# Kernel optimization log

Hardware: AMD Instinct MI355X
Metric: run time of the kernel (lower is better)

Reference implementation:

```python
import jax, jax.numpy as jnp
import numpy as np

SEQ, BATCH = 512, 32
VOCAB, HID, FF = 32000, 1024, 4096
HEADS, NX, MAXLEN = 8, 6, 512
EPS = 1e-5


def _full_layer_norm(t):
    # F.layer_norm(t, t.shape): normalize over ALL elements, no affine
    m = jnp.mean(t)
    v = jnp.mean((t - m) ** 2)
    return (t - m) * jax.lax.rsqrt(v + EPS)


def _attention(x, wq, bq, wk, bk, wv, bv, wo, bo):
    # x: [S, B, H]; faithful to the module's quirky reshape:
    # view(B, S//heads, heads, H) splits the SEQUENCE dim across heads,
    # each head keeps the full feature dim H; scores scaled by sqrt(H//heads).
    S, B, H = x.shape
    head_dim = H // HEADS
    q = x @ wq + bq
    k = x @ wk + bk
    v = x @ wv + bv

    def split(t):  # [S,B,H] -> [B, heads, S//heads, H]
        return t.transpose(1, 0, 2).reshape(B, S // HEADS, HEADS, H).transpose(0, 2, 1, 3)

    qh, kh, vh = split(q), split(k), split(v)
    energy = jnp.einsum('bhtf,bhsf->bhts', qh, kh) / np.sqrt(head_dim)
    att = jax.nn.softmax(energy, axis=-1)          # [B, heads, S//h, S//h]
    va = jnp.einsum('bhts,bhsf->bhtf', att, vh)    # [B, heads, S//h, H]
    va = va.transpose(2, 0, 1, 3).reshape(S, B, H)  # back to [S, B, H]
    return va @ wo + bo


def _sub_encoder(x, p, i):
    a = _attention(x, p['wq'][i], p['bq'][i], p['wk'][i], p['bk'][i],
                   p['wv'][i], p['bv'][i], p['wo'][i], p['bo'][i])
    mid = _full_layer_norm(a + x)
    f = jax.nn.relu(mid @ p['w1'][i] + p['b1'][i]) @ p['w2'][i] + p['b2'][i]
    return _full_layer_norm(mid + f)


def setup_inputs() -> dict:
    key = jax.random.key(0)
    ks = jax.random.split(key, 16)
    s = 0.02
    inp = {
        'x': jax.random.randint(ks[0], (SEQ, BATCH), 0, VOCAB),
        'emb': jax.random.normal(ks[1], (VOCAB, HID), jnp.float32) * s,
        'pos_emb': jax.random.normal(ks[2], (MAXLEN, HID), jnp.float32) * s,
        'wq': jax.random.normal(ks[3], (NX, HID, HID), jnp.float32) * s,
        'bq': jnp.zeros((NX, HID), jnp.float32),
        'wk': jax.random.normal(ks[4], (NX, HID, HID), jnp.float32) * s,
        'bk': jnp.zeros((NX, HID), jnp.float32),
        'wv': jax.random.normal(ks[5], (NX, HID, HID), jnp.float32) * s,
        'bv': jnp.zeros((NX, HID), jnp.float32),
        'wo': jax.random.normal(ks[6], (NX, HID, HID), jnp.float32) * s,
        'bo': jnp.zeros((NX, HID), jnp.float32),
        'w1': jax.random.normal(ks[7], (NX, HID, FF), jnp.float32) * s,
        'b1': jnp.zeros((NX, FF), jnp.float32),
        'w2': jax.random.normal(ks[8], (NX, FF, HID), jnp.float32) * s,
        'b2': jnp.zeros((NX, HID), jnp.float32),
    }
    return inp


def reference(x, emb, pos_emb, wq, bq, wk, bk, wv, bv, wo, bo, w1, b1, w2, b2):
    # dropout layers are identity (eval mode); src_mask=None path
    S = x.shape[0]
    p = dict(wq=wq, bq=bq, wk=wk, bk=bk, wv=wv, bv=bv, wo=wo, bo=bo,
             w1=w1, b1=b1, w2=w2, b2=b2)
    h = emb[x] * np.sqrt(HID) + pos_emb[jnp.arange(S)][:, None, :]
    for i in range(NX):
        h = _sub_encoder(h, p, i)
    return h
```

## Files before the change

### kernel.cpp

```cpp
#include <hip/hip_runtime.h>
#include <hip/hip_bf16.h>
#include <stdint.h>

typedef __bf16 bf16_t;
typedef __bf16 bf16x8 __attribute__((ext_vector_type(8)));
typedef __bf16 bf16x4 __attribute__((ext_vector_type(4)));
typedef float  f32x4  __attribute__((ext_vector_type(4)));
typedef float  f32x16 __attribute__((ext_vector_type(16)));

#define SEQ   512
#define BATCH 32
#define HID   1024
#define FFD   4096
#define NROW  (SEQ*BATCH)
#define NTOT  ((long)NROW*HID)
#define QKVS  3072

typedef __attribute__((address_space(3))) uint32_t lds_u32;
typedef __attribute__((address_space(1))) const uint32_t glb_u32;

__device__ __forceinline__ void gload_lds16(const void* g, void* l) {
  glb_u32* gp = reinterpret_cast<glb_u32*>(reinterpret_cast<uintptr_t>(g));
  lds_u32* lp = reinterpret_cast<lds_u32*>(reinterpret_cast<uintptr_t>(l));
  __builtin_amdgcn_global_load_lds(gp, lp, 16, 0, 0);
}

__global__ __launch_bounds__(256) void embed_k(const int* __restrict__ x,
    const float* __restrict__ emb, const float* __restrict__ pos,
    bf16_t* __restrict__ hb, float* __restrict__ stId)
{
  if (blockIdx.x == 0 && threadIdx.x == 0) { stId[0] = 0.f; stId[1] = 1.f; }
  const long row = blockIdx.x;
  const int  s   = (int)(row >> 5);
  const long idx = x[row];
  const int  t   = threadIdx.x;
  float4 e  = ((const float4*)(emb + idx*HID))[t];
  float4 pv = ((const float4*)(pos + (long)s*HID))[t];
  bf16x4 ob = {(bf16_t)(e.x*32.f+pv.x), (bf16_t)(e.y*32.f+pv.y),
               (bf16_t)(e.z*32.f+pv.z), (bf16_t)(e.w*32.f+pv.w)};
  *(bf16x4*)(hb + row*HID + (long)t*4) = ob;
}

__device__ __forceinline__ void wcvtNL_body(const float* __restrict__ W,
    bf16_t* __restrict__ wT, int K, int N, int bid)
{
  const int t  = threadIdx.x;
  const int nt = N >> 9;
  const int n  = ((bid % nt) << 9) + t;
  const int k0 = (bid / nt) << 6;
#pragma unroll
  for (int kb = 0; kb < 64; kb += 8) {
    bf16x8 o;
#pragma unroll
    for (int j = 0; j < 8; ++j)
      o[j] = (bf16_t)W[(long)(k0 + kb + j)*N + n];
    *(bf16x8*)&wT[(long)n*K + k0 + kb] = o;
  }
}

__device__ __forceinline__ void csum512_body(const float* __restrict__ W,
    float* __restrict__ out, int K, int N, int bid)
{
  const int n = bid*512 + threadIdx.x;
  float s0 = 0.f, s1 = 0.f, s2 = 0.f, s3 = 0.f;
  for (int k = 0; k < K; k += 4) {
    s0 += W[(long)k*N + n];
    s1 += W[(long)(k+1)*N + n];
    s2 += W[(long)(k+2)*N + n];
    s3 += W[(long)(k+3)*N + n];
  }
  out[n] = (s0 + s1) + (s2 + s3);
}

__global__ __launch_bounds__(512) void prep0(const float* __restrict__ wq,
    const float* __restrict__ wk, const float* __restrict__ wv,
    bf16_t* __restrict__ wT3, float* __restrict__ cs3)
{
  const int b = blockIdx.x;
  if (b < 96) {
    const int sel = b >> 5;
    const float* W = sel == 0 ? wq : sel == 1 ? wk : wv;
    wcvtNL_body(W, wT3 + (size_t)sel*HID*HID, HID, HID, b & 31);
  } else {
    const int col = (b - 96)*512 + threadIdx.x;
    const int sel = col >> 10, n = col & 1023;
    const float* W = sel == 0 ? wq : sel == 1 ? wk : wv;
    float s = 0.f;
    for (int k = 0; k < HID; ++k) s += W[(long)k*HID + n];
    cs3[col] = s;
  }
}

__global__ __launch_bounds__(512) void prep_k(
    const float* __restrict__ Wo, bf16_t* __restrict__ wTo,
    const float* __restrict__ W1, bf16_t* __restrict__ wT1, float* __restrict__ cs1,
    const float* __restrict__ W2, bf16_t* __restrict__ wT2,
    const float* __restrict__ Wq, const float* __restrict__ Wk,
    const float* __restrict__ Wv, bf16_t* __restrict__ wT3,
    float* __restrict__ cs3)
{
  const int b = blockIdx.x;
  if (b < 32)        wcvtNL_body(Wo, wTo, HID, HID, b);
  else if (b < 160)  wcvtNL_body(W1, wT1, HID, FFD, b - 32);
  else if (b < 288)  wcvtNL_body(W2, wT2, FFD, HID, b - 160);
  else if (b < 296)  csum512_body(W1, cs1, HID, FFD, b - 288);
  else if (b < 392) {
    const int i = b - 296, sel = i >> 5;
    const float* W = sel == 0 ? Wq : sel == 1 ? Wk : Wv;
    wcvtNL_body(W, wT3 + (size_t)sel*HID*HID, HID, HID, i & 31);
  } else {
    const int col = (b - 392)*512 + threadIdx.x;
    const int sel = col >> 10, n = col & 1023;
    const float* W = sel == 0 ? Wq : sel == 1 ? Wk : Wv;
    float s = 0.f;
    for (int k = 0; k < HID; ++k) s += W[(long)k*HID + n];
    cs3[col] = s;
  }
}

template<int MODE>
__global__ __launch_bounds__(512, 4)
void gemmW(const bf16_t* __restrict__ A, const bf16_t* __restrict__ Bt,
           const float* __restrict__ ba, const float* __restrict__ bb,
           const float* __restrict__ bc, const float* __restrict__ cs,
           const float* __restrict__ stats, const bf16_t* __restrict__ res,
           bf16_t* __restrict__ outB, float* __restrict__ part,
           int M, int N, int K)
{
  __shared__ bf16_t As[128][64];
  __shared__ bf16_t Bs[256][64];
  __shared__ float  rs[512], rq[512];
  const int tid = threadIdx.x;
  const int w = tid >> 6, l = tid & 63;
  const int wm = w >> 2, wn = w & 3;
  const int lr = l & 31, hi = l >> 5;

  const int nbn = N >> 8;
  const int nwg = gridDim.x;
  const int q8 = nwg >> 3, r8 = nwg & 7;
  const int xcd = blockIdx.x & 7, bidx = blockIdx.x >> 3;
  const int wg = (xcd < r8 ? xcd*(q8+1) : r8*(q8+1) + (xcd-r8)*q8) + bidx;
  const long bm = wg / nbn, bn = wg % nbn;
  const long rA0 = bm << 7, rB0 = bn << 8;

  const int srow   = tid >> 3;
  const int schunk = (((tid & 7) ^ ((tid >> 3) & 7)) << 3);
  const int ldsw   = (tid >> 6) << 10;

  f32x16 a00 = {0}, a01 = {0}, a10 = {0}, a11 = {0};

#define STG_TILE(kt) do { \
    const long kb_ = (long)(kt)*64 + schunk; \
    gload_lds16(A  + (rA0 + srow)*(long)K + kb_,        (char*)As + ldsw); \
    gload_lds16(A  + (rA0 + 64 + srow)*(long)K + kb_,   (char*)As + 8192 + ldsw); \
    gload_lds16(Bt + (rB0 + srow)*(long)K + kb_,        (char*)Bs + ldsw); \
    gload_lds16(Bt + (rB0 + 64 + srow)*(long)K + kb_,   (char*)Bs + 8192 + ldsw); \
    gload_lds16(Bt + (rB0 + 128 + srow)*(long)K + kb_,  (char*)Bs + 16384 + ldsw); \
    gload_lds16(Bt + (rB0 + 192 + srow)*(long)K + kb_,  (char*)Bs + 24576 + ldsw); \
  } while (0)
#define FRA(mt, kk) (*(const bf16x8*)((const char*)As + (wm*64 + (mt)*32 + lr)*128 + \
                      ((((kk)*2 + hi) ^ (l & 7)) << 4)))
#define FRB(nt, kk) (*(const bf16x8*)((const char*)Bs + (wn*64 + (nt)*32 + lr)*128 + \
                      ((((kk)*2 + hi) ^ (l & 7)) << 4)))

  const int nk = K >> 6;
  for (int t = 0; t < nk; ++t) {
    __syncthreads();
    STG_TILE(t);
    __syncthreads();
#pragma unroll
    for (int kk = 0; kk < 4; ++kk) {
      bf16x8 fa0 = FRA(0, kk), fa1 = FRA(1, kk);
      bf16x8 fb0 = FRB(0, kk), fb1 = FRB(1, kk);
      a00 = __builtin_amdgcn_mfma_f32_32x32x16_bf16(fa0, fb0, a00, 0, 0, 0);
      a01 = __builtin_amdgcn_mfma_f32_32x32x16_bf16(fa0, fb1, a01, 0, 0, 0);
      a10 = __builtin_amdgcn_mfma_f32_32x32x16_bf16(fa1, fb0, a10, 0, 0, 0);
      a11 = __builtin_amdgcn_mfma_f32_32x32x16_bf16(fa1, fb1, a11, 0, 0, 0);
    }
  }
#undef STG_TILE
#undef FRA
#undef FRB

  const float mS = stats[0], rS = stats[1];
  const bool q3 = (N == 3072);
  float ls = 0.f, lsq = 0.f;
  const long rowT = rA0 + wm*64 + 4*hi;
  const long colT = rB0 + wn*64 + lr;
#pragma unroll
  for (int nt = 0; nt < 2; ++nt) {
    const long col = colT + nt*32;
    float bv;
    if (MODE == 3 && q3)
      bv = col < 1024 ? ba[col] : col < 2048 ? bb[col - 1024] : bc[col - 2048];
    else
      bv = ba[col];
    float beta = 0.f;
    if (MODE == 3 || MODE == 4) beta = bv - mS*rS*cs[col];
#pragma unroll
    for (int mt = 0; mt < 2; ++mt) {
      const f32x16 acc = mt == 0 ? (nt == 0 ? a00 : a01) : (nt == 0 ? a10 : a11);
#pragma unroll
      for (int r = 0; r < 16; ++r) {
        const long row = rowT + mt*32 + (r & 3) + 8*(r >> 2);
        const long off = row*(long)N + col;
        float v;
        if (MODE == 3)      v = fmaf(acc[r], rS, beta);
        else if (MODE == 4) v = fmaxf(fmaf(acc[r], rS, beta), 0.f);
        else {
          v = acc[r] + bv + ((float)res[off] - mS)*rS;
          ls += v; lsq += v*v;
        }
        outB[off] = (bf16_t)v;
      }
    }
  }
  if (MODE == 5) {
    rs[tid] = ls; rq[tid] = lsq;
    __syncthreads();
    for (int o = 256; o > 0; o >>= 1) {
      if (tid < o) { rs[tid] += rs[tid+o]; rq[tid] += rq[tid+o]; }
      __syncthreads();
    }
    if (tid == 0) { part[2*blockIdx.x] = rs[0]; part[2*blockIdx.x + 1] = rq[0]; }
  }
}

__global__ __launch_bounds__(256) void attn_m(
    const bf16_t* __restrict__ qkv, bf16_t* __restrict__ ob)
{
  __shared__ __align__(16) bf16_t QK[2][8192];
  __shared__ __align__(16) bf16_t Ps[64*64];
  bf16_t* Vs = &QK[0][0];
  bf16_t* Os = &QK[1][0];

  const int tid = threadIdx.x;
  const int w = tid >> 6, l = tid & 63;
  const int fr = l & 15, kq = l >> 4;
  const int head = blockIdx.x & 7, b = blockIdx.x >> 3;
  const long rbase = (long)head*32 + b;

  const int lr  = tid >> 2;
  const int sslot = (tid & 15) ^ (tid >> 4);

  f32x4 accS[4] = {{0,0,0,0},{0,0,0,0},{0,0,0,0},{0,0,0,0}};

  for (int kc = 0; kc < HID; kc += 128) {
    __syncthreads();
#pragma unroll
    for (int i = 0; i < 4; ++i) {
      const int r = i*16 + (tid >> 4);
      const long gq = ((long)r*256 + rbase)*QKVS + kc + sslot*8;
      gload_lds16(qkv + gq,        (char*)&QK[0][0] + i*4096 + w*1024);
      gload_lds16(qkv + gq + 1024, (char*)&QK[1][0] + i*4096 + w*1024);
    }
    __syncthreads();
#pragma unroll
    for (int kk = 0; kk < 4; ++kk) {
      const int ra = w*16 + fr;
      bf16x8 a = *(const bf16x8*)&QK[0][ra*128 + (((kk*4 + kq) ^ fr) << 3)];
#pragma unroll
      for (int n = 0; n < 4; ++n) {
        const int rb = n*16 + fr;
        bf16x8 bv = *(const bf16x8*)&QK[1][rb*128 + (((kk*4 + kq) ^ fr) << 3)];
        accS[n] = __builtin_amdgcn_mfma_f32_16x16x32_bf16(a, bv, accS[n], 0, 0, 0);
      }
    }
  }

  const float scale = 0.08838834764831843f;
  float pj[4][4];
#pragma unroll
  for (int j = 0; j < 4; ++j) {
    float m = fmaxf(fmaxf(accS[0][j], accS[1][j]), fmaxf(accS[2][j], accS[3][j]));
    m = fmaxf(m, __shfl_xor(m, 1));
    m = fmaxf(m, __shfl_xor(m, 2));
    m = fmaxf(m, __shfl_xor(m, 4));
    m = fmaxf(m, __shfl_xor(m, 8));
    m *= scale;
    float s = 0.f;
#pragma unroll
    for (int n = 0; n < 4; ++n) { pj[n][j] = __expf(accS[n][j]*scale - m); s += pj[n][j]; }
    s += __shfl_xor(s, 1);
    s += __shfl_xor(s, 2);
    s += __shfl_xor(s, 4);
    s += __shfl_xor(s, 8);
    const float rv = 1.f / s;
#pragma unroll
    for (int n = 0; n < 4; ++n) pj[n][j] *= rv;
  }
#pragma unroll
  for (int n = 0; n < 4; ++n)
#pragma unroll
    for (int j = 0; j < 4; ++j) {
      const int r = w*16 + kq*4 + j;
      const int cpos = n*16 + fr;
      Ps[r*64 + (((cpos >> 3) ^ (r & 7)) << 3) + (cpos & 7)] = (bf16_t)pj[n][j];
    }
  __syncthreads();

  const long orow = (long)lr*256 + b*8 + head;
  for (int fc = 0; fc < HID; fc += 128) {
    const bf16_t* vrow = qkv + ((long)lr*256 + rbase)*QKVS + 2048 + fc;
#pragma unroll
    for (int i = 0; i < 4; ++i) {
      const int f0 = (tid & 3)*8 + i*32;
      uint4 vv = *(const uint4*)&vrow[f0];
      const bf16_t* ve = (const bf16_t*)&vv;
#pragma unroll
      for (int j = 0; j < 8; ++j) {
        const int f = f0 + j;
        Vs[f*64 + (((lr >> 3) ^ (f & 7)) << 3) + (lr & 7)] = ve[j];
      }
    }
    __syncthreads();
    const int ra = w*16 + fr;
    bf16x8 a0 = *(const bf16x8*)&Ps[ra*64 + ((kq       ^ (ra & 7)) << 3)];
    bf16x8 a1 = *(const bf16x8*)&Ps[ra*64 + (((4 + kq) ^ (ra & 7)) << 3)];
    f32x4 accO[8];
#pragma unroll
    for (int nt = 0; nt < 8; ++nt) {
      const int f = nt*16 + fr;
      bf16x8 b0 = *(const bf16x8*)&Vs[f*64 + ((kq       ^ (f & 7)) << 3)];
      bf16x8 b1 = *(const bf16x8*)&Vs[f*64 + (((4 + kq) ^ (f & 7)) << 3)];
      accO[nt] = __builtin_amdgcn_mfma_f32_16x16x32_bf16(a0, b0, (f32x4){0.f,0.f,0.f,0.f}, 0, 0, 0);
      accO[nt] = __builtin_amdgcn_mfma_f32_16x16x32_bf16(a1, b1, accO[nt], 0, 0, 0);
    }
#pragma unroll
    for (int nt = 0; nt < 8; ++nt)
#pragma unroll
      for (int j = 0; j < 4; ++j) {
        const int r = w*16 + kq*4 + j;
        const int cpos = nt*16 + fr;
        Os[r*128 + (((cpos >> 3) ^ (r & 7)) << 3) + (cpos & 7)] = (bf16_t)accO[nt][j];
      }
    __syncthreads();
#pragma unroll
    for (int i = 0; i < 4; ++i) {
      const int p = (tid & 3)*4 + i;
      uint4 vv = *(const uint4*)&Os[lr*128 + ((p ^ (lr & 7)) << 3)];
      *(uint4*)&ob[orow*HID + fc + p*8] = vv;
    }
  }
}

__global__ __launch_bounds__(256) void reduce2(const float* __restrict__ part,
                                               float* __restrict__ stats, int np)
{
  __shared__ double sh[256], sh2[256];
  const int tid = threadIdx.x;
  double s = 0.0, s2 = 0.0;
  for (int i = tid; i < np; i += 256) { s += part[2*i]; s2 += part[2*i + 1]; }
  sh[tid] = s; sh2[tid] = s2; __syncthreads();
  for (int o = 128; o > 0; o >>= 1) {
    if (tid < o) { sh[tid] += sh[tid+o]; sh2[tid] += sh2[tid+o]; }
    __syncthreads();
  }
  if (tid == 0) {
    const double n = (double)NTOT;
    const double mean = sh[0] / n;
    const double var  = sh2[0] / n - mean*mean;
    stats[0] = (float)mean;
    stats[1] = (float)(1.0 / sqrt(var + 1e-5));
  }
}

__global__ __launch_bounds__(256) void final_norm(const bf16_t* __restrict__ t,
    const float* __restrict__ stats, float* __restrict__ out)
{
  const float m = stats[0], r = stats[1];
  const long n8 = NTOT / 8;
  for (long i = (long)blockIdx.x*blockDim.x + threadIdx.x; i < n8;
       i += (long)gridDim.x*blockDim.x) {
    bf16x8 v = ((const bf16x8*)t)[i];
    float4 o0 = {((float)v[0]-m)*r, ((float)v[1]-m)*r, ((float)v[2]-m)*r, ((float)v[3]-m)*r};
    float4 o1 = {((float)v[4]-m)*r, ((float)v[5]-m)*r, ((float)v[6]-m)*r, ((float)v[7]-m)*r};
    ((float4*)out)[2*i]   = o0;
    ((float4*)out)[2*i+1] = o1;
  }
}

extern "C" void kernel_launch(void* const* d_in, const int* in_sizes, int n_in,
                              void* d_out, int out_size, void* d_ws, size_t ws_size,
                              hipStream_t stream)
{
  const int*   x    = (const int*)  d_in[0];
  const float* emb  = (const float*)d_in[1];
  const float* pos  = (const float*)d_in[2];
  const float* wq_a = (const float*)d_in[3];
  const float* bq_a = (const float*)d_in[4];
  const float* wk_a = (const float*)d_in[5];
  const float* bk_a = (const float*)d_in[6];
  const float* wv_a = (const float*)d_in[7];
  const float* bv_a = (const float*)d_in[8];
  const float* wo_a = (const float*)d_in[9];
  const float* bo_a = (const float*)d_in[10];
  const float* w1_a = (const float*)d_in[11];
  const float* b1_a = (const float*)d_in[12];
  const float* w2_a = (const float*)d_in[13];
  const float* b2_a = (const float*)d_in[14];

  char* p = (char*)d_ws;
  auto take = [&](size_t n) { char* r = p; p += (n + 255) & ~(size_t)255; return r; };
  bf16_t* hb   = (bf16_t*)take(NTOT*2);
  bf16_t* U    = (bf16_t*)take((size_t)NROW*FFD*2);
  bf16_t* qkv  = U;
  bf16_t* attb = U + 3*NTOT;
  bf16_t* ffb  = U;
  bf16_t* wTo  = (bf16_t*)take((size_t)HID*HID*2);
  bf16_t* wT1  = (bf16_t*)take((size_t)HID*FFD*2);
  bf16_t* wT2  = (bf16_t*)take((size_t)HID*FFD*2);
  bf16_t* wT3  = (bf16_t*)take((size_t)3*HID*HID*2);
  float*  cs1  = (float*) take(FFD*4);
  float*  cs3  = (float*) take(QKVS*4);
  float*  part = (float*) take(4096*4);
  float*  stId = (float*) take(256);
  float*  st1  = (float*) take(256);
  float*  st2  = (float*) take(256);

  const int gQKV = (NROW/128)*(QKVS/256);
  const int gH   = (NROW/128)*(HID/256);
  const int gF   = (NROW/128)*(FFD/256);

  embed_k<<<NROW, 256, 0, stream>>>(x, emb, pos, hb, stId);
  prep0<<<102, 512, 0, stream>>>(wq_a, wk_a, wv_a, wT3, cs3);

  for (int i = 0; i < 6; ++i) {
    const float* Bq = bq_a + (size_t)i*HID;
    const float* Bk = bk_a + (size_t)i*HID;
    const float* Bv = bv_a + (size_t)i*HID;
    const float* Wo = wo_a + (size_t)i*HID*HID;  const float* Bo = bo_a + (size_t)i*HID;
    const float* W1 = w1_a + (size_t)i*HID*FFD;  const float* B1 = b1_a + (size_t)i*FFD;
    const float* W2 = w2_a + (size_t)i*FFD*HID;  const float* B2 = b2_a + (size_t)i*HID;
    const float* stIn = (i == 0) ? stId : st2;
    const int haveNext = (i < 5);
    const float* Wqn = wq_a + (size_t)(i+1)*HID*HID;
    const float* Wkn = wk_a + (size_t)(i+1)*HID*HID;
    const float* Wvn = wv_a + (size_t)(i+1)*HID*HID;

    gemmW<3><<<gQKV, 512, 0, stream>>>(hb, wT3, Bq, Bk, Bv, cs3, stIn,
                                       nullptr, qkv, nullptr, NROW, QKVS, HID);

    attn_m<<<256, 256, 0, stream>>>(qkv, attb);

    prep_k<<<haveNext ? 398 : 296, 512, 0, stream>>>(
        Wo, wTo, W1, wT1, cs1, W2, wT2, Wqn, Wkn, Wvn, wT3, cs3);

    gemmW<5><<<gH, 512, 0, stream>>>(attb, wTo, Bo, Bo, Bo, nullptr, stIn,
                                     hb, hb, part, NROW, HID, HID);
    reduce2<<<1, 256, 0, stream>>>(part, st1, gH);

    gemmW<4><<<gF, 512, 0, stream>>>(hb, wT1, B1, B1, B1, cs1, st1,
                                     nullptr, ffb, nullptr, NROW, FFD, HID);

    gemmW<5><<<gH, 512, 0, stream>>>(ffb, wT2, B2, B2, B2, nullptr, st1,
                                     hb, hb, part, NROW, HID, FFD);
    reduce2<<<1, 256, 0, stream>>>(part, st2, gH);
  }

  final_norm<<<2048, 256, 0, stream>>>(hb, st2, (float*)d_out);
}
```

Measured before the change: 3.452 ms.

## Fold norm-stat reduction into GEMM epilogues and double-buffer attention loads

Removes the single-block reduce2 kernels. Every consumer GEMM and the final norm now reduce the per-block partial sums themselves, which cuts twelve tiny serial launches at the cost of redundant reductions in every block. The attention kernel double-buffers its Q/K LDS staging using explicit vmcnt waits and raw barriers. It also prefetches V rows into registers one chunk ahead, so memory latency overlaps with MFMA work. Separate part1/part2 buffers keep the reads of the input stats from clashing with the writes of new partials.

```diff
diff --git a/kernel.cpp b/kernel.cpp
--- a/kernel.cpp
+++ b/kernel.cpp
@@ -24,12 +24,12 @@
   lds_u32* lp = reinterpret_cast<lds_u32*>(reinterpret_cast<uintptr_t>(l));
   __builtin_amdgcn_global_load_lds(gp, lp, 16, 0, 0);
 }
+#define BAR() asm volatile("s_barrier" ::: "memory")
 
 __global__ __launch_bounds__(256) void embed_k(const int* __restrict__ x,
     const float* __restrict__ emb, const float* __restrict__ pos,
-    bf16_t* __restrict__ hb, float* __restrict__ stId)
-{
-  if (blockIdx.x == 0 && threadIdx.x == 0) { stId[0] = 0.f; stId[1] = 1.f; }
+    bf16_t* __restrict__ hb)
+{
   const long row = blockIdx.x;
   const int  s   = (int)(row >> 5);
   const long idx = x[row];
@@ -39,6 +39,27 @@
   bf16x4 ob = {(bf16_t)(e.x*32.f+pv.x), (bf16_t)(e.y*32.f+pv.y),
                (bf16_t)(e.z*32.f+pv.z), (bf16_t)(e.w*32.f+pv.w)};
   *(bf16x4*)(hb + row*HID + (long)t*4) = ob;
+}
+
+__device__ __forceinline__ void stats_reduce(const float* __restrict__ part,
+    int np, double* shd, float& mS, float& rS, int nthr)
+{
+  if (np == 0) { mS = 0.f; rS = 1.f; return; }
+  const int tid = threadIdx.x;
+  double s = 0.0, s2 = 0.0;
+  for (int i = tid; i < np; i += nthr) { s += (double)part[2*i]; s2 += (double)part[2*i+1]; }
+#pragma unroll
+  for (int o = 1; o < 64; o <<= 1) { s += __shfl_xor(s, o); s2 += __shfl_xor(s2, o); }
+  __syncthreads();
+  const int w = tid >> 6, nw = nthr >> 6;
+  if ((tid & 63) == 0) { shd[w] = s; shd[8 + w] = s2; }
+  __syncthreads();
+  double ts = 0.0, ts2 = 0.0;
+  for (int i = 0; i < nw; ++i) { ts += shd[i]; ts2 += shd[8 + i]; }
+  const double mean = ts / (double)NTOT;
+  const double var  = ts2 / (double)NTOT - mean*mean;
+  mS = (float)mean;
+  rS = (float)(1.0 / sqrt(var + 1e-5));
 }
 
 __device__ __forceinline__ void wcvtNL_body(const float* __restrict__ W,
@@ -123,7 +144,8 @@
 void gemmW(const bf16_t* __restrict__ A, const bf16_t* __restrict__ Bt,
            const float* __restrict__ ba, const float* __restrict__ bb,
            const float* __restrict__ bc, const float* __restrict__ cs,
-           const float* __restrict__ stats, const bf16_t* __restrict__ res,
+           const float* __restrict__ partIn, int npIn,
+           const bf16_t* __restrict__ res,
            bf16_t* __restrict__ outB, float* __restrict__ part,
            int M, int N, int K)
 {
@@ -182,7 +204,9 @@
 #undef FRA
 #undef FRB
 
-  const float mS = stats[0], rS = stats[1];
+  float mS, rS;
+  stats_reduce(partIn, npIn, (double*)&As[0][0], mS, rS, 512);
+
   const bool q3 = (N == 3072);
   float ls = 0.f, lsq = 0.f;
   const long rowT = rA0 + wm*64 + 4*hi;
@@ -229,10 +253,11 @@
 __global__ __launch_bounds__(256) void attn_m(
     const bf16_t* __restrict__ qkv, bf16_t* __restrict__ ob)
 {
-  __shared__ __align__(16) bf16_t QK[2][8192];
-  __shared__ __align__(16) bf16_t Ps[64*64];
-  bf16_t* Vs = &QK[0][0];
-  bf16_t* Os = &QK[1][0];
+  __shared__ __align__(16) bf16_t Qb[2][8192];
+  __shared__ __align__(16) bf16_t Kb[2][8192];
+  __shared__ __align__(16) bf16_t Ps[4096];
+  bf16_t* Vs = &Qb[0][0];
+  bf16_t* Os = &Kb[0][0];
 
   const int tid = threadIdx.x;
   const int w = tid >> 6, l = tid & 63;
@@ -245,28 +270,39 @@
 
   f32x4 accS[4] = {{0,0,0,0},{0,0,0,0},{0,0,0,0},{0,0,0,0}};
 
-  for (int kc = 0; kc < HID; kc += 128) {
-    __syncthreads();
-#pragma unroll
-    for (int i = 0; i < 4; ++i) {
-      const int r = i*16 + (tid >> 4);
-      const long gq = ((long)r*256 + rbase)*QKVS + kc + sslot*8;
-      gload_lds16(qkv + gq,        (char*)&QK[0][0] + i*4096 + w*1024);
-      gload_lds16(qkv + gq + 1024, (char*)&QK[1][0] + i*4096 + w*1024);
-    }
-    __syncthreads();
+#define STAGE_QK(qb, kb, kc) do { \
+    _Pragma("unroll") for (int i_ = 0; i_ < 4; ++i_) { \
+      const int r_ = i_*16 + (tid >> 4); \
+      const long gq_ = ((long)r_*256 + rbase)*QKVS + (kc) + sslot*8; \
+      gload_lds16(qkv + gq_,        (char*)(qb) + i_*4096 + w*1024); \
+      gload_lds16(qkv + gq_ + 1024, (char*)(kb) + i_*4096 + w*1024); \
+    } } while (0)
+
+  STAGE_QK(Qb[0], Kb[0], 0);
+#pragma unroll
+  for (int c = 0; c < 8; ++c) {
+    const int cur = c & 1;
+    if (c < 7) {
+      STAGE_QK(Qb[cur ^ 1], Kb[cur ^ 1], (c + 1)*128);
+      asm volatile("s_waitcnt vmcnt(8)" ::: "memory");
+    } else {
+      asm volatile("s_waitcnt vmcnt(0)" ::: "memory");
+    }
+    BAR();
 #pragma unroll
     for (int kk = 0; kk < 4; ++kk) {
       const int ra = w*16 + fr;
-      bf16x8 a = *(const bf16x8*)&QK[0][ra*128 + (((kk*4 + kq) ^ fr) << 3)];
+      bf16x8 a = *(const bf16x8*)&Qb[cur][ra*128 + (((kk*4 + kq) ^ fr) << 3)];
 #pragma unroll
       for (int n = 0; n < 4; ++n) {
         const int rb = n*16 + fr;
-        bf16x8 bv = *(const bf16x8*)&QK[1][rb*128 + (((kk*4 + kq) ^ fr) << 3)];
+        bf16x8 bv = *(const bf16x8*)&Kb[cur][rb*128 + (((kk*4 + kq) ^ fr) << 3)];
         accS[n] = __builtin_amdgcn_mfma_f32_16x16x32_bf16(a, bv, accS[n], 0, 0, 0);
       }
     }
-  }
+    BAR();
+  }
+#undef STAGE_QK
 
   const float scale = 0.08838834764831843f;
   float pj[4][4];
@@ -300,13 +336,22 @@
   __syncthreads();
 
   const long orow = (long)lr*256 + b*8 + head;
-  for (int fc = 0; fc < HID; fc += 128) {
-    const bf16_t* vrow = qkv + ((long)lr*256 + rbase)*QKVS + 2048 + fc;
+  const bf16_t* vbase = qkv + ((long)lr*256 + rbase)*QKVS + 2048;
+  const int ra2 = w*16 + fr;
+  bf16x8 a0 = *(const bf16x8*)&Ps[ra2*64 + ((kq       ^ (ra2 & 7)) << 3)];
+  bf16x8 a1 = *(const bf16x8*)&Ps[ra2*64 + (((4 + kq) ^ (ra2 & 7)) << 3)];
+
+  uint4 vr[4];
+#pragma unroll
+  for (int i = 0; i < 4; ++i)
+    vr[i] = *(const uint4*)&vbase[(tid & 3)*8 + i*32];
+
+#pragma unroll
+  for (int fc8 = 0; fc8 < 8; ++fc8) {
 #pragma unroll
     for (int i = 0; i < 4; ++i) {
       const int f0 = (tid & 3)*8 + i*32;
-      uint4 vv = *(const uint4*)&vrow[f0];
-      const bf16_t* ve = (const bf16_t*)&vv;
+      const bf16_t* ve = (const bf16_t*)&vr[i];
 #pragma unroll
       for (int j = 0; j < 8; ++j) {
         const int f = f0 + j;
@@ -314,9 +359,11 @@
       }
     }
     __syncthreads();
-    const int ra = w*16 + fr;
-    bf16x8 a0 = *(const bf16x8*)&Ps[ra*64 + ((kq       ^ (ra & 7)) << 3)];
-    bf16x8 a1 = *(const bf16x8*)&Ps[ra*64 + (((4 + kq) ^ (ra & 7)) << 3)];
+    if (fc8 < 7) {
+#pragma unroll
+      for (int i = 0; i < 4; ++i)
+        vr[i] = *(const uint4*)&vbase[(fc8 + 1)*128 + (tid & 3)*8 + i*32];
+    }
     f32x4 accO[8];
 #pragma unroll
     for (int nt = 0; nt < 8; ++nt) {
@@ -339,36 +386,17 @@
     for (int i = 0; i < 4; ++i) {
       const int p = (tid & 3)*4 + i;
       uint4 vv = *(const uint4*)&Os[lr*128 + ((p ^ (lr & 7)) << 3)];
-      *(uint4*)&ob[orow*HID + fc + p*8] = vv;
-    }
-  }
-}
-
-__global__ __launch_bounds__(256) void reduce2(const float* __restrict__ part,
-                                               float* __restrict__ stats, int np)
-{
-  __shared__ double sh[256], sh2[256];
-  const int tid = threadIdx.x;
-  double s = 0.0, s2 = 0.0;
-  for (int i = tid; i < np; i += 256) { s += part[2*i]; s2 += part[2*i + 1]; }
-  sh[tid] = s; sh2[tid] = s2; __syncthreads();
-  for (int o = 128; o > 0; o >>= 1) {
-    if (tid < o) { sh[tid] += sh[tid+o]; sh2[tid] += sh2[tid+o]; }
-    __syncthreads();
-  }
-  if (tid == 0) {
-    const double n = (double)NTOT;
-    const double mean = sh[0] / n;
-    const double var  = sh2[0] / n - mean*mean;
-    stats[0] = (float)mean;
-    stats[1] = (float)(1.0 / sqrt(var + 1e-5));
+      *(uint4*)&ob[orow*HID + fc8*128 + p*8] = vv;
+    }
   }
 }
 
 __global__ __launch_bounds__(256) void final_norm(const bf16_t* __restrict__ t,
-    const float* __restrict__ stats, float* __restrict__ out)
-{
-  const float m = stats[0], r = stats[1];
+    const float* __restrict__ part, int np, float* __restrict__ out)
+{
+  __shared__ double shd[16];
+  float m, r;
+  stats_reduce(part, np, shd, m, r, 256);
   const long n8 = NTOT / 8;
   for (long i = (long)blockIdx.x*blockDim.x + threadIdx.x; i < n8;
        i += (long)gridDim.x*blockDim.x) {
@@ -413,16 +441,14 @@
   bf16_t* wT3  = (bf16_t*)take((size_t)3*HID*HID*2);
   float*  cs1  = (float*) take(FFD*4);
   float*  cs3  = (float*) take(QKVS*4);
-  float*  part = (float*) take(4096*4);
-  float*  stId = (float*) take(256);
-  float*  st1  = (float*) take(256);
-  float*  st2  = (float*) take(256);
+  float*  part1= (float*) take(2048*4);
+  float*  part2= (float*) take(2048*4);
 
   const int gQKV = (NROW/128)*(QKVS/256);
   const int gH   = (NROW/128)*(HID/256);
   const int gF   = (NROW/128)*(FFD/256);
 
-  embed_k<<<NROW, 256, 0, stream>>>(x, emb, pos, hb, stId);
+  embed_k<<<NROW, 256, 0, stream>>>(x, emb, pos, hb);
   prep0<<<102, 512, 0, stream>>>(wq_a, wk_a, wv_a, wT3, cs3);
 
   for (int i = 0; i < 6; ++i) {
@@ -432,13 +458,13 @@
     const float* Wo = wo_a + (size_t)i*HID*HID;  const float* Bo = bo_a + (size_t)i*HID;
     const float* W1 = w1_a + (size_t)i*HID*FFD;  const float* B1 = b1_a + (size_t)i*FFD;
     const float* W2 = w2_a + (size_t)i*FFD*HID;  const float* B2 = b2_a + (size_t)i*HID;
-    const float* stIn = (i == 0) ? stId : st2;
+    const int npIn = (i == 0) ? 0 : gH;
     const int haveNext = (i < 5);
     const float* Wqn = wq_a + (size_t)(i+1)*HID*HID;
     const float* Wkn = wk_a + (size_t)(i+1)*HID*HID;
     const float* Wvn = wv_a + (size_t)(i+1)*HID*HID;
 
-    gemmW<3><<<gQKV, 512, 0, stream>>>(hb, wT3, Bq, Bk, Bv, cs3, stIn,
+    gemmW<3><<<gQKV, 512, 0, stream>>>(hb, wT3, Bq, Bk, Bv, cs3, part2, npIn,
                                        nullptr, qkv, nullptr, NROW, QKVS, HID);
 
     attn_m<<<256, 256, 0, stream>>>(qkv, attb);
@@ -446,17 +472,15 @@
     prep_k<<<haveNext ? 398 : 296, 512, 0, stream>>>(
         Wo, wTo, W1, wT1, cs1, W2, wT2, Wqn, Wkn, Wvn, wT3, cs3);
 
-    gemmW<5><<<gH, 512, 0, stream>>>(attb, wTo, Bo, Bo, Bo, nullptr, stIn,
-                                     hb, hb, part, NROW, HID, HID);
-    reduce2<<<1, 256, 0, stream>>>(part, st1, gH);
-
-    gemmW<4><<<gF, 512, 0, stream>>>(hb, wT1, B1, B1, B1, cs1, st1,
+    gemmW<5><<<gH, 512, 0, stream>>>(attb, wTo, Bo, Bo, Bo, nullptr, part2, npIn,
+                                     hb, hb, part1, NROW, HID, HID);
+
+    gemmW<4><<<gF, 512, 0, stream>>>(hb, wT1, B1, B1, B1, cs1, part1, gH,
                                      nullptr, ffb, nullptr, NROW, FFD, HID);
 
-    gemmW<5><<<gH, 512, 0, stream>>>(ffb, wT2, B2, B2, B2, nullptr, st1,
-                                     hb, hb, part, NROW, HID, FFD);
-    reduce2<<<1, 256, 0, stream>>>(part, st2, gH);
-  }
-
-  final_norm<<<2048, 256, 0, stream>>>(hb, st2, (float*)d_out);
-}
+    gemmW<5><<<gH, 512, 0, stream>>>(ffb, wT2, B2, B2, B2, nullptr, part1, gH,
+                                     hb, hb, part2, NROW, HID, FFD);
+  }
+
+  final_norm<<<2048, 256, 0, stream>>>(hb, part2, gH, (float*)d_out);
+}
```

New measurement: 3.405 ms. About the same (-1.3%).
